# Optimization experiments

Measured on AMD Instinct MI355X. Metric: run time of the kernel, lower is better.

## Reference

```python
import jax, jax.numpy as jnp
import numpy as np


def setup_inputs() -> dict:
    key = jax.random.key(0)
    ks = jax.random.split(key, 13)
    B, D, H, O = 4096, 2048, 3, 1  # batch, input_dim, hidden layer count, output_dim
    f32 = jnp.float32
    scale = 1.0 / np.sqrt(D)
    return {
        "x": jax.random.normal(ks[0], (B, D), f32),
        "w_mu_h": jax.random.normal(ks[1], (H, D, D), f32) * scale,
        "w_rho_h": jax.random.normal(ks[2], (H, D, D), f32) - 5.0,  # softplus(-5) ~ small std
        "b_mu_h": jax.random.normal(ks[3], (H, D), f32) * scale,
        "b_rho_h": jax.random.normal(ks[4], (H, D), f32) - 5.0,
        "w_mu_o": jax.random.normal(ks[5], (O, D), f32) * scale,
        "w_rho_o": jax.random.normal(ks[6], (O, D), f32) - 5.0,
        "b_mu_o": jax.random.normal(ks[7], (O,), f32) * scale,
        "b_rho_o": jax.random.normal(ks[8], (O,), f32) - 5.0,
        # reparameterization noise (torch.randn_like), passed explicitly for determinism
        "eps_w_h": jax.random.normal(ks[9], (H, D, D), f32),
        "eps_b_h": jax.random.normal(ks[10], (H, D), f32),
        "eps_w_o": jax.random.normal(ks[11], (O, D), f32),
        "eps_b_o": jax.random.normal(ks[12], (O,), f32),
    }


def _vlinear(x, w_mu, w_rho, b_mu, b_rho, eps_w, eps_b):
    # weight = mu + eps * softplus(rho); F.linear(x, W, b) = x @ W.T + b
    w = w_mu + eps_w * jax.nn.softplus(w_rho)
    b = b_mu + eps_b * jax.nn.softplus(b_rho)
    return x @ w.T + b


def reference(x, w_mu_h, w_rho_h, b_mu_h, b_rho_h,
              w_mu_o, w_rho_o, b_mu_o, b_rho_o,
              eps_w_h, eps_b_h, eps_w_o, eps_b_o):
    def step(h, p):
        wm, wr, bm, br, ew, eb = p
        h = jax.nn.relu(_vlinear(h, wm, wr, bm, br, ew, eb))
        return h, None

    h, _ = jax.lax.scan(step, x, (w_mu_h, w_rho_h, b_mu_h, b_rho_h, eps_w_h, eps_b_h))
    return _vlinear(h, w_mu_o, w_rho_o, b_mu_o, b_rho_o, eps_w_o, eps_b_o)
```

## Files before the change

### kernel.cpp

```cpp
#include <hip/hip_runtime.h>

#define BB 4096
#define DD 2048

typedef float f32x4 __attribute__((ext_vector_type(4)));
typedef __bf16 bf16x8 __attribute__((ext_vector_type(8)));

typedef __attribute__((address_space(1))) unsigned int gl_u32;
typedef __attribute__((address_space(3))) unsigned int lds_u32;

#define GLOAD_LDS16(gptr, sptr) \
  __builtin_amdgcn_global_load_lds((gl_u32*)(void*)(gptr), (lds_u32*)(sptr), 16, 0, 0)

__device__ __forceinline__ unsigned short f2bf(float f) {
  unsigned int u = __float_as_uint(f);
  u += 0x7fffu + ((u >> 16) & 1u);
  return (unsigned short)(u >> 16);
}

__device__ __forceinline__ float sp(float x) {
  float t = __expf(-fabsf(x));
  return fmaxf(x, 0.0f) + __logf(1.0f + t);
}

__device__ __forceinline__ void prep_w_vec4(
    const float* __restrict__ mu, const float* __restrict__ rho,
    const float* __restrict__ eps, unsigned short* __restrict__ Wh,
    long long i)
{
  float4 m = ((const float4*)mu)[i];
  float4 r = ((const float4*)rho)[i];
  float4 e = ((const float4*)eps)[i];
  ushort4 o;
  o.x = f2bf(m.x + e.x * sp(r.x));
  o.y = f2bf(m.y + e.y * sp(r.y));
  o.z = f2bf(m.z + e.z * sp(r.z));
  o.w = f2bf(m.w + e.w * sp(r.w));
  ((ushort4*)Wh)[i] = o;
}

__device__ __forceinline__ void prep_f32_vec4(
    const float* __restrict__ mu, const float* __restrict__ rho,
    const float* __restrict__ eps, float* __restrict__ out, long long i)
{
  float4 m = ((const float4*)mu)[i];
  float4 r = ((const float4*)rho)[i];
  float4 e = ((const float4*)eps)[i];
  float4 o;
  o.x = m.x + e.x * sp(r.x);
  o.y = m.y + e.y * sp(r.y);
  o.z = m.z + e.z * sp(r.z);
  o.w = m.w + e.w * sp(r.w);
  ((float4*)out)[i] = o;
}

__global__ __launch_bounds__(512) void prep0_kernel(
    const float* __restrict__ x,
    const float* __restrict__ wmuh, const float* __restrict__ wrhoh,
    const float* __restrict__ bmuh, const float* __restrict__ brhoh,
    const float* __restrict__ epswh, const float* __restrict__ epsbh,
    unsigned short* __restrict__ Wh, unsigned short* __restrict__ Xb,
    float* __restrict__ bh)
{
  const int b = blockIdx.x;
  const int t = threadIdx.x;
  if (b < 512) {
    long long base = (long long)b * 2048 + t;
    #pragma unroll
    for (int j = 0; j < 4; ++j)
      prep_w_vec4(wmuh, wrhoh, epswh, Wh, base + j * 512);
    return;
  }
  if (b < 1536) {
    long long base = (long long)(b - 512) * 2048 + t;
    #pragma unroll
    for (int j = 0; j < 4; ++j) {
      float4 v = ((const float4*)x)[base + j * 512];
      ushort4 o;
      o.x = f2bf(v.x); o.y = f2bf(v.y); o.z = f2bf(v.z); o.w = f2bf(v.w);
      ((ushort4*)Xb)[base + j * 512] = o;
    }
    return;
  }
  prep_f32_vec4(bmuh, brhoh, epsbh, bh, t);
}

#define NGEMM 512

struct GemmCoords { int m0, n0, mw, nw; int srow[2], sgc[2]; };

__device__ __forceinline__ GemmCoords gemm_coords(int id, int t) {
  GemmCoords g;
  const int w = t >> 6;
  const int p = id & 7;
  const int i4 = id >> 3;
  const int mt = (p & 3) * 8 + (i4 & 7);
  const int nt = (p >> 2) * 8 + (i4 >> 3);
  g.m0 = mt * 128;
  g.n0 = nt * 128;
  g.mw = (w >> 2) * 64;
  g.nw = (w & 3) * 32;
  #pragma unroll
  for (int i = 0; i < 2; ++i) {
    int c = i * 512 + t;
    g.srow[i] = c >> 3;
    g.sgc[i] = (c & 7) ^ (g.srow[i] & 7);
  }
  return g;
}

__device__ __forceinline__ void gemm_mainloop(
    const unsigned short* __restrict__ A,
    const unsigned short* __restrict__ W,
    unsigned short* sA, unsigned short* sB,
    const GemmCoords& gc, int t, f32x4 (&acc)[4][2])
{
  const int K = DD;
  const int l = t & 63;
  const int lq = l >> 4;
  const int lr = l & 15;
  for (int kt = 0; kt < K; kt += 64) {
    #pragma unroll
    for (int i = 0; i < 2; ++i) {
      int c = i * 512 + t;
      const unsigned short* ga = A + (size_t)(gc.m0 + gc.srow[i]) * K + kt + gc.sgc[i] * 8;
      GLOAD_LDS16(ga, &sA[c * 8]);
      const unsigned short* gb = W + (size_t)(gc.n0 + gc.srow[i]) * K + kt + gc.sgc[i] * 8;
      GLOAD_LDS16(gb, &sB[c * 8]);
    }
    __syncthreads();

    #pragma unroll
    for (int s = 0; s < 2; ++s) {
      bf16x8 af[4], bfr[2];
      int g = s * 4 + lq;
      #pragma unroll
      for (int i = 0; i < 4; ++i) {
        int ra = gc.mw + i * 16 + lr;
        af[i] = *(const bf16x8*)&sA[ra * 64 + (g ^ (ra & 7)) * 8];
      }
      #pragma unroll
      for (int j = 0; j < 2; ++j) {
        int rb = gc.nw + j * 16 + lr;
        bfr[j] = *(const bf16x8*)&sB[rb * 64 + (g ^ (rb & 7)) * 8];
      }
      #pragma unroll
      for (int i = 0; i < 4; ++i)
        #pragma unroll
        for (int j = 0; j < 2; ++j)
          acc[i][j] = __builtin_amdgcn_mfma_f32_16x16x32_bf16(af[i], bfr[j], acc[i][j], 0, 0, 0);
    }
    __syncthreads();
  }
}

__device__ __forceinline__ void gemm_epilogue_store(
    const GemmCoords& gc, int t, f32x4 (&acc)[4][2],
    const float* __restrict__ bias, unsigned short* __restrict__ C)
{
  const int N = DD;
  const int l = t & 63;
  const int lq = l >> 4;
  const int lr = l & 15;
  #pragma unroll
  for (int j = 0; j < 2; ++j) {
    int n = gc.n0 + gc.nw + j * 16 + lr;
    float bv = bias[n];
    #pragma unroll
    for (int i = 0; i < 4; ++i) {
      int mbase = gc.m0 + gc.mw + i * 16 + lq * 4;
      #pragma unroll
      for (int r = 0; r < 4; ++r) {
        float v = fmaxf(acc[i][j][r] + bv, 0.0f);
        C[(size_t)(mbase + r) * N + n] = f2bf(v);
      }
    }
  }
}

__global__ __launch_bounds__(512, 4) void gemm_relu_fused_kernel(
    const unsigned short* __restrict__ A,
    const unsigned short* __restrict__ W,
    const float* __restrict__ bias,
    unsigned short* __restrict__ C,
    const float* __restrict__ wmuh, const float* __restrict__ wrhoh,
    const float* __restrict__ bmuh, const float* __restrict__ brhoh,
    const float* __restrict__ wmuo, const float* __restrict__ wrhoo,
    const float* __restrict__ epswh, const float* __restrict__ epsbh,
    const float* __restrict__ epswo,
    unsigned short* __restrict__ Wh, float* __restrict__ bh,
    float* __restrict__ wo)
{
  __shared__ unsigned short sA[128 * 64];
  __shared__ unsigned short sB[128 * 64];

  const int id = blockIdx.x;
  const int t = threadIdx.x;

  if (id >= NGEMM) {
    const int pb = id - NGEMM;
    if (pb < 1024) {
      long long base = 1048576LL + (long long)pb * 2048 + t;
      #pragma unroll
      for (int j = 0; j < 4; ++j)
        prep_w_vec4(wmuh, wrhoh, epswh, Wh, base + j * 512);
      return;
    }
    #pragma unroll
    for (int j = 0; j < 2; ++j)
      prep_f32_vec4(bmuh, brhoh, epsbh, bh, 512 + j * 512 + t);
    prep_f32_vec4(wmuo, wrhoo, epswo, wo, t);
    return;
  }

  GemmCoords gc = gemm_coords(id, t);
  f32x4 acc[4][2] = {};
  gemm_mainloop(A, W, sA, sB, gc, t, acc);
  gemm_epilogue_store(gc, t, acc, bias, C);
}

__global__ __launch_bounds__(512, 4) void gemm_relu_kernel(
    const unsigned short* __restrict__ A,
    const unsigned short* __restrict__ W,
    const float* __restrict__ bias,
    unsigned short* __restrict__ C)
{
  __shared__ unsigned short sA[128 * 64];
  __shared__ unsigned short sB[128 * 64];
  const int t = threadIdx.x;
  GemmCoords gc = gemm_coords(blockIdx.x, t);
  f32x4 acc[4][2] = {};
  gemm_mainloop(A, W, sA, sB, gc, t, acc);
  gemm_epilogue_store(gc, t, acc, bias, C);
}

__global__ __launch_bounds__(512, 4) void gemm_relu_dot_kernel(
    const unsigned short* __restrict__ A,
    const unsigned short* __restrict__ W,
    const float* __restrict__ bias,
    const float* __restrict__ wo,
    float* __restrict__ Pbuf)
{
  __shared__ unsigned short sA[128 * 64];
  __shared__ unsigned short sB[128 * 64];
  const int t = threadIdx.x;

  GemmCoords gc = gemm_coords(blockIdx.x, t);
  f32x4 acc[4][2] = {};
  gemm_mainloop(A, W, sA, sB, gc, t, acc);

  const int l = t & 63;
  const int w = t >> 6;
  const int lq = l >> 4;
  const int lr = l & 15;
  const int nq = w & 3;

  float bv[2], wv[2];
  #pragma unroll
  for (int j = 0; j < 2; ++j) {
    int n = gc.n0 + gc.nw + j * 16 + lr;
    bv[j] = bias[n];
    wv[j] = wo[n];
  }
  float partial[4][4];
  #pragma unroll
  for (int i = 0; i < 4; ++i)
    #pragma unroll
    for (int r = 0; r < 4; ++r)
      partial[i][r] = fmaxf(acc[i][0][r] + bv[0], 0.0f) * wv[0]
                    + fmaxf(acc[i][1][r] + bv[1], 0.0f) * wv[1];

  #pragma unroll
  for (int d = 1; d <= 8; d <<= 1)
    #pragma unroll
    for (int i = 0; i < 4; ++i)
      #pragma unroll
      for (int r = 0; r < 4; ++r)
        partial[i][r] += __shfl_xor(partial[i][r], d, 64);

  float* sRed = (float*)sA;
  if (lr == 0) {
    #pragma unroll
    for (int i = 0; i < 4; ++i)
      #pragma unroll
      for (int r = 0; r < 4; ++r) {
        int row = gc.mw + i * 16 + lq * 4 + r;
        sRed[row * 4 + nq] = partial[i][r];
      }
  }
  __syncthreads();
  if (t < 128) {
    float s = sRed[t * 4 + 0] + sRed[t * 4 + 1] + sRed[t * 4 + 2] + sRed[t * 4 + 3];
    int nt = gc.n0 >> 7;
    Pbuf[nt * BB + gc.m0 + t] = s;
  }
}

__global__ __launch_bounds__(256) void reduce_out_kernel(
    const float* __restrict__ Pbuf,
    const float* __restrict__ bmuo, const float* __restrict__ brhoo,
    const float* __restrict__ epsbo,
    float* __restrict__ out)
{
  const int m = blockIdx.x * 256 + threadIdx.x;
  float s = bmuo[0] + epsbo[0] * sp(brhoo[0]);
  #pragma unroll
  for (int nt = 0; nt < 16; ++nt)
    s += Pbuf[nt * BB + m];
  out[m] = s;
}

extern "C" void kernel_launch(void* const* d_in, const int* in_sizes, int n_in,
                              void* d_out, int out_size, void* d_ws, size_t ws_size,
                              hipStream_t stream) {
  const float* x     = (const float*)d_in[0];
  const float* wmuh  = (const float*)d_in[1];
  const float* wrhoh = (const float*)d_in[2];
  const float* bmuh  = (const float*)d_in[3];
  const float* brhoh = (const float*)d_in[4];
  const float* wmuo  = (const float*)d_in[5];
  const float* wrhoo = (const float*)d_in[6];
  const float* bmuo  = (const float*)d_in[7];
  const float* brhoo = (const float*)d_in[8];
  const float* epswh = (const float*)d_in[9];
  const float* epsbh = (const float*)d_in[10];
  const float* epswo = (const float*)d_in[11];
  const float* epsbo = (const float*)d_in[12];

  char* ws = (char*)d_ws;
  unsigned short* Wh = (unsigned short*)(ws);
  unsigned short* Xb = (unsigned short*)(ws + 25165824);
  unsigned short* Ha = (unsigned short*)(ws + 25165824 + 16777216);
  unsigned short* Hb = (unsigned short*)(ws + 25165824 + 2 * 16777216);
  float* bh   = (float*)(ws + 25165824 + 3 * 16777216);
  float* wo   = (float*)(ws + 25165824 + 3 * 16777216 + 24576);
  float* Pbuf = (float*)(ws + 25165824 + 3 * 16777216 + 24576 + 8192);

  prep0_kernel<<<1537, 512, 0, stream>>>(
      x, wmuh, wrhoh, bmuh, brhoh, epswh, epsbh, Wh, Xb, bh);

  gemm_relu_fused_kernel<<<NGEMM + 1025, 512, 0, stream>>>(
      Xb, Wh, bh, Ha,
      wmuh, wrhoh, bmuh, brhoh, wmuo, wrhoo,
      epswh, epsbh, epswo, Wh, bh, wo);

  gemm_relu_kernel<<<NGEMM, 512, 0, stream>>>(Ha, Wh + 1 * 4194304, bh + DD, Hb);

  gemm_relu_dot_kernel<<<NGEMM, 512, 0, stream>>>(
      Hb, Wh + 2 * 4194304, bh + 2 * DD, wo, Pbuf);

  reduce_out_kernel<<<BB / 256, 256, 0, stream>>>(
      Pbuf, bmuo, brhoo, epsbo, (float*)d_out);
}
```

Before: 298.6 us.

## Merge all stages into one persistent kernel with grid barriers

```diff
diff --git a/kernel.cpp b/kernel.cpp
--- a/kernel.cpp
+++ b/kernel.cpp
@@ -54,38 +54,23 @@
   ((float4*)out)[i] = o;
 }
 
-__global__ __launch_bounds__(512) void prep0_kernel(
-    const float* __restrict__ x,
-    const float* __restrict__ wmuh, const float* __restrict__ wrhoh,
-    const float* __restrict__ bmuh, const float* __restrict__ brhoh,
-    const float* __restrict__ epswh, const float* __restrict__ epsbh,
-    unsigned short* __restrict__ Wh, unsigned short* __restrict__ Xb,
-    float* __restrict__ bh)
-{
-  const int b = blockIdx.x;
-  const int t = threadIdx.x;
-  if (b < 512) {
-    long long base = (long long)b * 2048 + t;
-    #pragma unroll
-    for (int j = 0; j < 4; ++j)
-      prep_w_vec4(wmuh, wrhoh, epswh, Wh, base + j * 512);
-    return;
-  }
-  if (b < 1536) {
-    long long base = (long long)(b - 512) * 2048 + t;
-    #pragma unroll
-    for (int j = 0; j < 4; ++j) {
-      float4 v = ((const float4*)x)[base + j * 512];
-      ushort4 o;
-      o.x = f2bf(v.x); o.y = f2bf(v.y); o.z = f2bf(v.z); o.w = f2bf(v.w);
-      ((ushort4*)Xb)[base + j * 512] = o;
-    }
-    return;
-  }
-  prep_f32_vec4(bmuh, brhoh, epsbh, bh, t);
-}
-
-#define NGEMM 512
+__device__ __forceinline__ void grid_barrier(unsigned* bar, unsigned nb) {
+  __syncthreads();
+  if (threadIdx.x == 0) {
+    __builtin_amdgcn_fence(__ATOMIC_RELEASE, "agent");
+    unsigned v = __hip_atomic_fetch_add(bar, 1u, __ATOMIC_ACQ_REL,
+                                        __HIP_MEMORY_SCOPE_AGENT);
+    unsigned target = (v / nb + 1u) * nb;
+    long long spins = 0;
+    while ((int)(__hip_atomic_load(bar, __ATOMIC_RELAXED,
+                                   __HIP_MEMORY_SCOPE_AGENT) - target) < 0) {
+      __builtin_amdgcn_s_sleep(8);
+      if (++spins > (1LL << 21)) break;
+    }
+    __builtin_amdgcn_fence(__ATOMIC_ACQUIRE, "agent");
+  }
+  __syncthreads();
+}
 
 struct GemmCoords { int m0, n0, mw, nw; int srow[2], sgc[2]; };
 
@@ -178,18 +163,30 @@
   }
 }
 
-__global__ __launch_bounds__(512, 4) void gemm_relu_fused_kernel(
-    const unsigned short* __restrict__ A,
-    const unsigned short* __restrict__ W,
-    const float* __restrict__ bias,
-    unsigned short* __restrict__ C,
+__device__ __forceinline__ void prep_w_share(
+    const float* __restrict__ wmuh, const float* __restrict__ wrhoh,
+    const float* __restrict__ epswh, unsigned short* __restrict__ Wh,
+    long long layer_base_vec4, int id, int t)
+{
+  long long base = layer_base_vec4 + (long long)id * 2048 + t;
+  #pragma unroll
+  for (int j = 0; j < 4; ++j)
+    prep_w_vec4(wmuh, wrhoh, epswh, Wh, base + j * 512);
+}
+
+__global__ __launch_bounds__(512, 4) void mega_kernel(
+    const float* __restrict__ x,
     const float* __restrict__ wmuh, const float* __restrict__ wrhoh,
     const float* __restrict__ bmuh, const float* __restrict__ brhoh,
     const float* __restrict__ wmuo, const float* __restrict__ wrhoo,
+    const float* __restrict__ bmuo, const float* __restrict__ brhoo,
     const float* __restrict__ epswh, const float* __restrict__ epsbh,
-    const float* __restrict__ epswo,
-    unsigned short* __restrict__ Wh, float* __restrict__ bh,
-    float* __restrict__ wo)
+    const float* __restrict__ epswo, const float* __restrict__ epsbo,
+    unsigned short* __restrict__ Wh, unsigned short* __restrict__ Xb,
+    unsigned short* __restrict__ Ha, unsigned short* __restrict__ Hb,
+    float* __restrict__ bh, float* __restrict__ wo,
+    float* __restrict__ Pbuf, float* __restrict__ out,
+    unsigned* __restrict__ bar)
 {
   __shared__ unsigned short sA[128 * 64];
   __shared__ unsigned short sB[128 * 64];
@@ -197,117 +194,119 @@
   const int id = blockIdx.x;
   const int t = threadIdx.x;
 
-  if (id >= NGEMM) {
-    const int pb = id - NGEMM;
-    if (pb < 1024) {
-      long long base = 1048576LL + (long long)pb * 2048 + t;
-      #pragma unroll
-      for (int j = 0; j < 4; ++j)
-        prep_w_vec4(wmuh, wrhoh, epswh, Wh, base + j * 512);
-      return;
-    }
-    #pragma unroll
-    for (int j = 0; j < 2; ++j)
-      prep_f32_vec4(bmuh, brhoh, epsbh, bh, 512 + j * 512 + t);
-    prep_f32_vec4(wmuo, wrhoo, epswo, wo, t);
-    return;
-  }
-
-  GemmCoords gc = gemm_coords(id, t);
-  f32x4 acc[4][2] = {};
-  gemm_mainloop(A, W, sA, sB, gc, t, acc);
-  gemm_epilogue_store(gc, t, acc, bias, C);
-}
-
-__global__ __launch_bounds__(512, 4) void gemm_relu_kernel(
-    const unsigned short* __restrict__ A,
-    const unsigned short* __restrict__ W,
-    const float* __restrict__ bias,
-    unsigned short* __restrict__ C)
-{
-  __shared__ unsigned short sA[128 * 64];
-  __shared__ unsigned short sB[128 * 64];
-  const int t = threadIdx.x;
-  GemmCoords gc = gemm_coords(blockIdx.x, t);
-  f32x4 acc[4][2] = {};
-  gemm_mainloop(A, W, sA, sB, gc, t, acc);
-  gemm_epilogue_store(gc, t, acc, bias, C);
-}
-
-__global__ __launch_bounds__(512, 4) void gemm_relu_dot_kernel(
-    const unsigned short* __restrict__ A,
-    const unsigned short* __restrict__ W,
-    const float* __restrict__ bias,
-    const float* __restrict__ wo,
-    float* __restrict__ Pbuf)
-{
-  __shared__ unsigned short sA[128 * 64];
-  __shared__ unsigned short sB[128 * 64];
-  const int t = threadIdx.x;
-
-  GemmCoords gc = gemm_coords(blockIdx.x, t);
-  f32x4 acc[4][2] = {};
-  gemm_mainloop(A, W, sA, sB, gc, t, acc);
-
-  const int l = t & 63;
-  const int w = t >> 6;
-  const int lq = l >> 4;
-  const int lr = l & 15;
-  const int nq = w & 3;
-
-  float bv[2], wv[2];
-  #pragma unroll
-  for (int j = 0; j < 2; ++j) {
-    int n = gc.n0 + gc.nw + j * 16 + lr;
-    bv[j] = bias[n];
-    wv[j] = wo[n];
-  }
-  float partial[4][4];
-  #pragma unroll
-  for (int i = 0; i < 4; ++i)
-    #pragma unroll
-    for (int r = 0; r < 4; ++r)
-      partial[i][r] = fmaxf(acc[i][0][r] + bv[0], 0.0f) * wv[0]
-                    + fmaxf(acc[i][1][r] + bv[1], 0.0f) * wv[1];
-
-  #pragma unroll
-  for (int d = 1; d <= 8; d <<= 1)
+  {
+    long long wb = (long long)id * 2048 + t;
+    #pragma unroll
+    for (int j = 0; j < 4; ++j)
+      prep_w_vec4(wmuh, wrhoh, epswh, Wh, wb + j * 512);
+    long long xb = (long long)id * 4096 + t;
+    #pragma unroll
+    for (int j = 0; j < 8; ++j) {
+      float4 v = ((const float4*)x)[xb + j * 512];
+      ushort4 o;
+      o.x = f2bf(v.x); o.y = f2bf(v.y); o.z = f2bf(v.z); o.w = f2bf(v.w);
+      ((ushort4*)Xb)[xb + j * 512] = o;
+    }
+    if (id == 0) prep_f32_vec4(bmuh, brhoh, epsbh, bh, t);
+  }
+  grid_barrier(bar, 512u);
+
+  const GemmCoords gc = gemm_coords(id, t);
+  const int role = (id >> 8) & 1;
+
+  {
+    if (role) {
+      prep_w_share(wmuh, wrhoh, epswh, Wh, 1048576LL, id, t);
+      if (id == 256) prep_f32_vec4(bmuh, brhoh, epsbh, bh, 512 + t);
+    }
+    f32x4 acc[4][2] = {};
+    gemm_mainloop(Xb, Wh, sA, sB, gc, t, acc);
+    gemm_epilogue_store(gc, t, acc, bh, Ha);
+    if (!role) {
+      prep_w_share(wmuh, wrhoh, epswh, Wh, 1048576LL, id, t);
+      if (id == 0) prep_f32_vec4(bmuh, brhoh, epsbh, bh, 512 + t);
+    }
+  }
+  grid_barrier(bar, 512u);
+
+  {
+    if (role) {
+      prep_w_share(wmuh, wrhoh, epswh, Wh, 2097152LL, id, t);
+      if (id == 256) prep_f32_vec4(bmuh, brhoh, epsbh, bh, 1024 + t);
+      if (id == 257) prep_f32_vec4(wmuo, wrhoo, epswo, wo, t);
+    }
+    f32x4 acc[4][2] = {};
+    gemm_mainloop(Ha, Wh + 1 * 4194304, sA, sB, gc, t, acc);
+    gemm_epilogue_store(gc, t, acc, bh + DD, Hb);
+    if (!role) {
+      prep_w_share(wmuh, wrhoh, epswh, Wh, 2097152LL, id, t);
+      if (id == 0) prep_f32_vec4(bmuh, brhoh, epsbh, bh, 1024 + t);
+      if (id == 1) prep_f32_vec4(wmuo, wrhoo, epswo, wo, t);
+    }
+  }
+  grid_barrier(bar, 512u);
+
+  {
+    f32x4 acc[4][2] = {};
+    gemm_mainloop(Hb, Wh + 2 * 4194304, sA, sB, gc, t, acc);
+
+    const int l = t & 63;
+    const int w = t >> 6;
+    const int lq = l >> 4;
+    const int lr = l & 15;
+    const int nq = w & 3;
+    const float* bias = bh + 2 * DD;
+
+    float bv[2], wv[2];
+    #pragma unroll
+    for (int j = 0; j < 2; ++j) {
+      int n = gc.n0 + gc.nw + j * 16 + lr;
+      bv[j] = bias[n];
+      wv[j] = wo[n];
+    }
+    float partial[4][4];
     #pragma unroll
     for (int i = 0; i < 4; ++i)
       #pragma unroll
       for (int r = 0; r < 4; ++r)
-        partial[i][r] += __shfl_xor(partial[i][r], d, 64);
-
-  float* sRed = (float*)sA;
-  if (lr == 0) {
-    #pragma unroll
-    for (int i = 0; i < 4; ++i)
-      #pragma unroll
-      for (int r = 0; r < 4; ++r) {
-        int row = gc.mw + i * 16 + lq * 4 + r;
-        sRed[row * 4 + nq] = partial[i][r];
-      }
-  }
-  __syncthreads();
-  if (t < 128) {
-    float s = sRed[t * 4 + 0] + sRed[t * 4 + 1] + sRed[t * 4 + 2] + sRed[t * 4 + 3];
-    int nt = gc.n0 >> 7;
-    Pbuf[nt * BB + gc.m0 + t] = s;
-  }
-}
-
-__global__ __launch_bounds__(256) void reduce_out_kernel(
-    const float* __restrict__ Pbuf,
-    const float* __restrict__ bmuo, const float* __restrict__ brhoo,
-    const float* __restrict__ epsbo,
-    float* __restrict__ out)
-{
-  const int m = blockIdx.x * 256 + threadIdx.x;
-  float s = bmuo[0] + epsbo[0] * sp(brhoo[0]);
-  #pragma unroll
-  for (int nt = 0; nt < 16; ++nt)
-    s += Pbuf[nt * BB + m];
-  out[m] = s;
+        partial[i][r] = fmaxf(acc[i][0][r] + bv[0], 0.0f) * wv[0]
+                      + fmaxf(acc[i][1][r] + bv[1], 0.0f) * wv[1];
+
+    #pragma unroll
+    for (int d = 1; d <= 8; d <<= 1)
+      #pragma unroll
+      for (int i = 0; i < 4; ++i)
+        #pragma unroll
+        for (int r = 0; r < 4; ++r)
+          partial[i][r] += __shfl_xor(partial[i][r], d, 64);
+
+    float* sRed = (float*)sA;
+    if (lr == 0) {
+      #pragma unroll
+      for (int i = 0; i < 4; ++i)
+        #pragma unroll
+        for (int r = 0; r < 4; ++r) {
+          int row = gc.mw + i * 16 + lq * 4 + r;
+          sRed[row * 4 + nq] = partial[i][r];
+        }
+    }
+    __syncthreads();
+    if (t < 128) {
+      float s = sRed[t * 4 + 0] + sRed[t * 4 + 1] + sRed[t * 4 + 2] + sRed[t * 4 + 3];
+      int nt = gc.n0 >> 7;
+      Pbuf[nt * BB + gc.m0 + t] = s;
+    }
+  }
+  grid_barrier(bar, 512u);
+
+  if (id < 8) {
+    int m = id * 512 + t;
+    float s = bmuo[0] + epsbo[0] * sp(brhoo[0]);
+    #pragma unroll
+    for (int nt = 0; nt < 16; ++nt)
+      s += Pbuf[nt * BB + m];
+    out[m] = s;
+  }
 }
 
 extern "C" void kernel_launch(void* const* d_in, const int* in_sizes, int n_in,
@@ -335,20 +334,12 @@
   float* bh   = (float*)(ws + 25165824 + 3 * 16777216);
   float* wo   = (float*)(ws + 25165824 + 3 * 16777216 + 24576);
   float* Pbuf = (float*)(ws + 25165824 + 3 * 16777216 + 24576 + 8192);
-
-  prep0_kernel<<<1537, 512, 0, stream>>>(
-      x, wmuh, wrhoh, bmuh, brhoh, epswh, epsbh, Wh, Xb, bh);
-
-  gemm_relu_fused_kernel<<<NGEMM + 1025, 512, 0, stream>>>(
-      Xb, Wh, bh, Ha,
-      wmuh, wrhoh, bmuh, brhoh, wmuo, wrhoo,
-      epswh, epsbh, epswo, Wh, bh, wo);
-
-  gemm_relu_kernel<<<NGEMM, 512, 0, stream>>>(Ha, Wh + 1 * 4194304, bh + DD, Hb);
-
-  gemm_relu_dot_kernel<<<NGEMM, 512, 0, stream>>>(
-      Hb, Wh + 2 * 4194304, bh + 2 * DD, wo, Pbuf);
-
-  reduce_out_kernel<<<BB / 256, 256, 0, stream>>>(
-      Pbuf, bmuo, brhoo, epsbo, (float*)d_out);
-}
+  unsigned* bar = (unsigned*)(ws + 25165824 + 3 * 16777216 + 24576 + 8192 + 262144);
+
+  hipMemsetAsync(bar, 0, 64, stream);
+
+  mega_kernel<<<512, 512, 0, stream>>>(
+      x, wmuh, wrhoh, bmuh, brhoh, wmuo, wrhoo, bmuo, brhoo,
+      epswh, epsbh, epswo, epsbo,
+      Wh, Xb, Ha, Hb, bh, wo, Pbuf, (float*)d_out, bar);
+}
```

New measurement: 513.7 us. +72.0%, slower.

## Use 256x128 GEMM tiles with triple-buffered async LDS pipeline

Applied to the files above, without the earlier changes.

```diff
diff --git a/kernel.cpp b/kernel.cpp
--- a/kernel.cpp
+++ b/kernel.cpp
@@ -11,6 +11,9 @@
 
 #define GLOAD_LDS16(gptr, sptr) \
   __builtin_amdgcn_global_load_lds((gl_u32*)(void*)(gptr), (lds_u32*)(sptr), 16, 0, 0)
+
+#define SBAR_MEM() asm volatile("s_barrier" ::: "memory")
+#define VMCNT(n)   asm volatile("s_waitcnt vmcnt(" #n ")" ::: "memory")
 
 __device__ __forceinline__ unsigned short f2bf(float f) {
   unsigned int u = __float_as_uint(f);
@@ -85,23 +88,22 @@
   prep_f32_vec4(bmuh, brhoh, epsbh, bh, t);
 }
 
-#define NGEMM 512
-
-struct GemmCoords { int m0, n0, mw, nw; int srow[2], sgc[2]; };
-
-__device__ __forceinline__ GemmCoords gemm_coords(int id, int t) {
-  GemmCoords g;
-  const int w = t >> 6;
+#define NGEMM 256
+#define ATILE 16384
+#define BUFE  24576
+
+struct Coords256 { int m0, n0; int srow[4], sgc[4]; };
+
+__device__ __forceinline__ Coords256 coords256(int id, int t) {
+  Coords256 g;
   const int p = id & 7;
   const int i4 = id >> 3;
-  const int mt = (p & 3) * 8 + (i4 & 7);
-  const int nt = (p >> 2) * 8 + (i4 >> 3);
-  g.m0 = mt * 128;
+  const int mt = (p & 3) * 4 + (i4 & 3);
+  const int nt = (p >> 2) * 8 + (i4 >> 2);
+  g.m0 = mt * 256;
   g.n0 = nt * 128;
-  g.mw = (w >> 2) * 64;
-  g.nw = (w & 3) * 32;
-  #pragma unroll
-  for (int i = 0; i < 2; ++i) {
+  #pragma unroll
+  for (int i = 0; i < 4; ++i) {
     int c = i * 512 + t;
     g.srow[i] = c >> 3;
     g.sgc[i] = (c & 7) ^ (g.srow[i] & 7);
@@ -109,76 +111,101 @@
   return g;
 }
 
-__device__ __forceinline__ void gemm_mainloop(
-    const unsigned short* __restrict__ A,
-    const unsigned short* __restrict__ W,
-    unsigned short* sA, unsigned short* sB,
-    const GemmCoords& gc, int t, f32x4 (&acc)[4][2])
-{
-  const int K = DD;
-  const int l = t & 63;
-  const int lq = l >> 4;
-  const int lr = l & 15;
-  for (int kt = 0; kt < K; kt += 64) {
-    #pragma unroll
-    for (int i = 0; i < 2; ++i) {
-      int c = i * 512 + t;
-      const unsigned short* ga = A + (size_t)(gc.m0 + gc.srow[i]) * K + kt + gc.sgc[i] * 8;
-      GLOAD_LDS16(ga, &sA[c * 8]);
-      const unsigned short* gb = W + (size_t)(gc.n0 + gc.srow[i]) * K + kt + gc.sgc[i] * 8;
-      GLOAD_LDS16(gb, &sB[c * 8]);
-    }
-    __syncthreads();
-
-    #pragma unroll
-    for (int s = 0; s < 2; ++s) {
-      bf16x8 af[4], bfr[2];
-      int g = s * 4 + lq;
-      #pragma unroll
-      for (int i = 0; i < 4; ++i) {
-        int ra = gc.mw + i * 16 + lr;
-        af[i] = *(const bf16x8*)&sA[ra * 64 + (g ^ (ra & 7)) * 8];
-      }
-      #pragma unroll
-      for (int j = 0; j < 2; ++j) {
-        int rb = gc.nw + j * 16 + lr;
-        bfr[j] = *(const bf16x8*)&sB[rb * 64 + (g ^ (rb & 7)) * 8];
-      }
-      #pragma unroll
-      for (int i = 0; i < 4; ++i)
-        #pragma unroll
-        for (int j = 0; j < 2; ++j)
-          acc[i][j] = __builtin_amdgcn_mfma_f32_16x16x32_bf16(af[i], bfr[j], acc[i][j], 0, 0, 0);
-    }
-    __syncthreads();
-  }
-}
-
-__device__ __forceinline__ void gemm_epilogue_store(
-    const GemmCoords& gc, int t, f32x4 (&acc)[4][2],
+__device__ __forceinline__ void stage_tile(
+    const unsigned short* __restrict__ A, const unsigned short* __restrict__ W,
+    unsigned short* buf, const Coords256& gc, int kt, int t)
+{
+  #pragma unroll
+  for (int i = 0; i < 4; ++i) {
+    int c = i * 512 + t;
+    const unsigned short* ga = A + (size_t)(gc.m0 + gc.srow[i]) * DD + kt + gc.sgc[i] * 8;
+    GLOAD_LDS16(ga, &buf[c * 8]);
+  }
+  #pragma unroll
+  for (int i = 0; i < 2; ++i) {
+    int c = i * 512 + t;
+    const unsigned short* gb = W + (size_t)(gc.n0 + gc.srow[i]) * DD + kt + gc.sgc[i] * 8;
+    GLOAD_LDS16(gb, &buf[ATILE + c * 8]);
+  }
+}
+
+__device__ __forceinline__ void compute_ktile(
+    const unsigned short* buf, int wm, int wn, int lq, int lr,
+    f32x4 (&acc)[4][4])
+{
+  #pragma unroll
+  for (int s = 0; s < 2; ++s) {
+    bf16x8 af[4], bfv[4];
+    const int g = s * 4 + lq;
+    const int go = (g ^ (lr & 7)) * 8;
+    #pragma unroll
+    for (int i = 0; i < 4; ++i) {
+      int ra = wm * 64 + i * 16 + lr;
+      af[i] = *(const bf16x8*)&buf[ra * 64 + go];
+    }
+    #pragma unroll
+    for (int j = 0; j < 4; ++j) {
+      int rb = wn * 64 + j * 16 + lr;
+      bfv[j] = *(const bf16x8*)&buf[ATILE + rb * 64 + go];
+    }
+    __builtin_amdgcn_s_setprio(1);
+    #pragma unroll
+    for (int i = 0; i < 4; ++i)
+      #pragma unroll
+      for (int j = 0; j < 4; ++j)
+        acc[i][j] = __builtin_amdgcn_mfma_f32_16x16x32_bf16(af[i], bfv[j], acc[i][j], 0, 0, 0);
+    __builtin_amdgcn_s_setprio(0);
+  }
+}
+
+__device__ __forceinline__ void gemm_mainloop256(
+    const unsigned short* __restrict__ A, const unsigned short* __restrict__ W,
+    unsigned short (*lds)[BUFE], const Coords256& gc, int t, f32x4 (&acc)[4][4])
+{
+  const int l = t & 63, lq = l >> 4, lr = l & 15;
+  const int w = t >> 6, wm = w & 3, wn = w >> 2;
+  unsigned short *p0 = lds[0], *p1 = lds[1], *p2 = lds[2];
+  stage_tile(A, W, p0, gc, 0, t);
+  stage_tile(A, W, p1, gc, 64, t);
+  for (int k = 0; k < 32; ++k) {
+    if (k < 30) {
+      stage_tile(A, W, p2, gc, (k + 2) * 64, t);
+      VMCNT(12);
+    } else if (k == 30) {
+      VMCNT(6);
+    } else {
+      VMCNT(0);
+    }
+    SBAR_MEM();
+    compute_ktile(p0, wm, wn, lq, lr, acc);
+    SBAR_MEM();
+    unsigned short* tmp = p0; p0 = p1; p1 = p2; p2 = tmp;
+  }
+}
+
+__device__ __forceinline__ void epilogue_store256(
+    const Coords256& gc, int t, f32x4 (&acc)[4][4],
     const float* __restrict__ bias, unsigned short* __restrict__ C)
 {
-  const int N = DD;
-  const int l = t & 63;
-  const int lq = l >> 4;
-  const int lr = l & 15;
-  #pragma unroll
-  for (int j = 0; j < 2; ++j) {
-    int n = gc.n0 + gc.nw + j * 16 + lr;
+  const int l = t & 63, lq = l >> 4, lr = l & 15;
+  const int w = t >> 6, wm = w & 3, wn = w >> 2;
+  #pragma unroll
+  for (int j = 0; j < 4; ++j) {
+    int n = gc.n0 + wn * 64 + j * 16 + lr;
     float bv = bias[n];
     #pragma unroll
     for (int i = 0; i < 4; ++i) {
-      int mbase = gc.m0 + gc.mw + i * 16 + lq * 4;
+      int mbase = gc.m0 + wm * 64 + i * 16 + lq * 4;
       #pragma unroll
       for (int r = 0; r < 4; ++r) {
         float v = fmaxf(acc[i][j][r] + bv, 0.0f);
-        C[(size_t)(mbase + r) * N + n] = f2bf(v);
+        C[(size_t)(mbase + r) * DD + n] = f2bf(v);
       }
     }
   }
 }
 
-__global__ __launch_bounds__(512, 4) void gemm_relu_fused_kernel(
+__global__ __launch_bounds__(512, 2) void gemm_relu_fused_kernel(
     const unsigned short* __restrict__ A,
     const unsigned short* __restrict__ W,
     const float* __restrict__ bias,
@@ -191,8 +218,7 @@
     unsigned short* __restrict__ Wh, float* __restrict__ bh,
     float* __restrict__ wo)
 {
-  __shared__ unsigned short sA[128 * 64];
-  __shared__ unsigned short sB[128 * 64];
+  __shared__ unsigned short lds[3][BUFE];
 
   const int id = blockIdx.x;
   const int t = threadIdx.x;
@@ -213,52 +239,47 @@
     return;
   }
 
-  GemmCoords gc = gemm_coords(id, t);
-  f32x4 acc[4][2] = {};
-  gemm_mainloop(A, W, sA, sB, gc, t, acc);
-  gemm_epilogue_store(gc, t, acc, bias, C);
-}
-
-__global__ __launch_bounds__(512, 4) void gemm_relu_kernel(
+  Coords256 gc = coords256(id, t);
+  f32x4 acc[4][4] = {};
+  gemm_mainloop256(A, W, lds, gc, t, acc);
+  epilogue_store256(gc, t, acc, bias, C);
+}
+
+__global__ __launch_bounds__(512, 2) void gemm_relu_kernel(
     const unsigned short* __restrict__ A,
     const unsigned short* __restrict__ W,
     const float* __restrict__ bias,
     unsigned short* __restrict__ C)
 {
-  __shared__ unsigned short sA[128 * 64];
-  __shared__ unsigned short sB[128 * 64];
+  __shared__ unsigned short lds[3][BUFE];
   const int t = threadIdx.x;
-  GemmCoords gc = gemm_coords(blockIdx.x, t);
-  f32x4 acc[4][2] = {};
-  gemm_mainloop(A, W, sA, sB, gc, t, acc);
-  gemm_epilogue_store(gc, t, acc, bias, C);
-}
-
-__global__ __launch_bounds__(512, 4) void gemm_relu_dot_kernel(
+  Coords256 gc = coords256(blockIdx.x, t);
+  f32x4 acc[4][4] = {};
+  gemm_mainloop256(A, W, lds, gc, t, acc);
+  epilogue_store256(gc, t, acc, bias, C);
+}
+
+__global__ __launch_bounds__(512, 2) void gemm_relu_dot_kernel(
     const unsigned short* __restrict__ A,
     const unsigned short* __restrict__ W,
     const float* __restrict__ bias,
     const float* __restrict__ wo,
     float* __restrict__ Pbuf)
 {
-  __shared__ unsigned short sA[128 * 64];
-  __shared__ unsigned short sB[128 * 64];
+  __shared__ unsigned short lds[3][BUFE];
   const int t = threadIdx.x;
 
-  GemmCoords gc = gemm_coords(blockIdx.x, t);
-  f32x4 acc[4][2] = {};
-  gemm_mainloop(A, W, sA, sB, gc, t, acc);
-
-  const int l = t & 63;
-  const int w = t >> 6;
-  const int lq = l >> 4;
-  const int lr = l & 15;
-  const int nq = w & 3;
-
-  float bv[2], wv[2];
-  #pragma unroll
-  for (int j = 0; j < 2; ++j) {
-    int n = gc.n0 + gc.nw + j * 16 + lr;
+  Coords256 gc = coords256(blockIdx.x, t);
+  f32x4 acc[4][4] = {};
+  gemm_mainloop256(A, W, lds, gc, t, acc);
+
+  const int l = t & 63, lq = l >> 4, lr = l & 15;
+  const int w = t >> 6, wm = w & 3, wn = w >> 2;
+
+  float bv[4], wv[4];
+  #pragma unroll
+  for (int j = 0; j < 4; ++j) {
+    int n = gc.n0 + wn * 64 + j * 16 + lr;
     bv[j] = bias[n];
     wv[j] = wo[n];
   }
@@ -266,9 +287,13 @@
   #pragma unroll
   for (int i = 0; i < 4; ++i)
     #pragma unroll
-    for (int r = 0; r < 4; ++r)
-      partial[i][r] = fmaxf(acc[i][0][r] + bv[0], 0.0f) * wv[0]
-                    + fmaxf(acc[i][1][r] + bv[1], 0.0f) * wv[1];
+    for (int r = 0; r < 4; ++r) {
+      float s = 0.0f;
+      #pragma unroll
+      for (int j = 0; j < 4; ++j)
+        s += fmaxf(acc[i][j][r] + bv[j], 0.0f) * wv[j];
+      partial[i][r] = s;
+    }
 
   #pragma unroll
   for (int d = 1; d <= 8; d <<= 1)
@@ -278,19 +303,19 @@
       for (int r = 0; r < 4; ++r)
         partial[i][r] += __shfl_xor(partial[i][r], d, 64);
 
-  float* sRed = (float*)sA;
+  float* sRed = (float*)lds;
   if (lr == 0) {
     #pragma unroll
     for (int i = 0; i < 4; ++i)
       #pragma unroll
       for (int r = 0; r < 4; ++r) {
-        int row = gc.mw + i * 16 + lq * 4 + r;
-        sRed[row * 4 + nq] = partial[i][r];
+        int row = wm * 64 + i * 16 + lq * 4 + r;
+        sRed[row * 2 + wn] = partial[i][r];
       }
   }
   __syncthreads();
-  if (t < 128) {
-    float s = sRed[t * 4 + 0] + sRed[t * 4 + 1] + sRed[t * 4 + 2] + sRed[t * 4 + 3];
+  if (t < 256) {
+    float s = sRed[t * 2 + 0] + sRed[t * 2 + 1];
     int nt = gc.n0 >> 7;
     Pbuf[nt * BB + gc.m0 + t] = s;
   }
```

Result: slower. 320.4 us (+7.3%).
